# Kernel optimization log

Measured on AMD Instinct MI355X. Metric: run time of the kernel, lower is better.

## Reference

```python
import jax, jax.numpy as jnp
import numpy as np

T, H, E, I, K, G, KG = 16384, 1024, 64, 768, 8, 8, 4


def setup_inputs() -> dict:
    key = jax.random.key(0)
    ks = jax.random.split(key, 6)
    return {
        "hidden_states": jax.random.normal(ks[0], (T, H), jnp.float32),
        "gate_weight": jax.random.normal(ks[1], (E, H), jnp.float32) * 0.02,
        "correction_bias": jax.random.normal(ks[2], (E,), jnp.float32) * 0.01,
        "w_gate": jax.random.normal(ks[3], (E, I, H), jnp.float32) * 0.02,
        "w_up": jax.random.normal(ks[4], (E, I, H), jnp.float32) * 0.02,
        "w_down": jax.random.normal(ks[5], (E, H, I), jnp.float32) * 0.02,
    }


def _grouped_topk(hidden, gate_w, bias, top_k=K, n_group=G, topk_group=KG, renormalize=True):
    # gate runs in fp32 (MoEGate.dtype = float32)
    logits = hidden.astype(jnp.float32) @ gate_w.T  # [T, E]
    scores = jax.nn.sigmoid(logits)  # noaux_tc uses sigmoid scores
    s_choice = scores + bias[None, :].astype(jnp.float32)
    t, e = scores.shape
    # group score = sum of top-2 biased scores within each group
    grouped = s_choice.reshape(t, n_group, e // n_group)
    top2, _ = jax.lax.top_k(grouped, 2)
    group_scores = top2.sum(-1)  # [T, G]
    _, gidx = jax.lax.top_k(group_scores, topk_group)  # [T, KG]
    gmask = jnp.zeros((t, n_group), jnp.float32).at[jnp.arange(t)[:, None], gidx].set(1.0)
    emask = jnp.repeat(gmask, e // n_group, axis=1)  # [T, E]
    masked = jnp.where(emask > 0, s_choice, -jnp.inf)
    _, topk_idx = jax.lax.top_k(masked, top_k)  # [T, K]
    # weights use the unbiased sigmoid scores
    topk_w = jnp.take_along_axis(scores, topk_idx, axis=1)
    if renormalize:
        topk_w = topk_w / (topk_w.sum(-1, keepdims=True) + 1e-20)
    # routed_scaling_factor = 1.0
    return topk_idx, topk_w


def reference(hidden_states, gate_weight, correction_bias, w_gate, w_up, w_down):
    t = hidden_states.shape[0]
    topk_idx, topk_w = _grouped_topk(hidden_states, gate_weight, correction_bias)
    # dense combine weights [T, E]: zero except at selected experts
    combine = jnp.zeros((t, E), hidden_states.dtype).at[
        jnp.arange(t)[:, None], topk_idx
    ].add(topk_w.astype(hidden_states.dtype))

    def step(acc, xs):
        wg, wu, wd, c = xs  # wg/wu: [I,H], wd: [H,I], c: [T]
        h = jax.nn.silu(hidden_states @ wg.T) * (hidden_states @ wu.T)  # [T, I]
        return acc + c[:, None] * (h @ wd.T), None

    acc0 = jnp.zeros_like(hidden_states)
    out, _ = jax.lax.scan(step, acc0, (w_gate, w_up, w_down, combine.T))
    return out
```

## Files before the change

kernel.cpp:

```cpp
#include <hip/hip_runtime.h>
#include <hip/hip_bf16.h>
#include <math.h>

#define T_TOK 16384
#define H_DIM 1024
#define E_NUM 64
#define I_DIM 768
#define TOPK  8
#define NGRP  8
#define KGRP  4
#define S_ASN (T_TOK*TOPK)
#define BM 128
#define BK 64
#define MAXBLK (S_ASN/BM + E_NUM)

typedef __attribute__((ext_vector_type(4))) float f4v;
typedef __attribute__((ext_vector_type(8))) short s8v;
typedef __attribute__((ext_vector_type(4))) unsigned short u4sv;

#define GLDS16(g, l) __builtin_amdgcn_global_load_lds( \
    (const __attribute__((address_space(1))) void*)(g), \
    (__attribute__((address_space(3))) void*)(l), 16, 0, 0)

static __device__ __forceinline__ short f2bf(float f){
  union { float f; unsigned u; } a; a.f = f;
  unsigned u = a.u;
  unsigned r = (u + 0x7fffu + ((u >> 16) & 1u)) >> 16;
  return (short)r;
}
static __device__ __forceinline__ float bf2f(unsigned short h){
  union { unsigned u; float f; } a; a.u = ((unsigned)h) << 16; return a.f;
}
static __device__ __forceinline__ s8v cvt8(f4v a, f4v b){
  s8v r;
  r[0]=f2bf(a[0]); r[1]=f2bf(a[1]); r[2]=f2bf(a[2]); r[3]=f2bf(a[3]);
  r[4]=f2bf(b[0]); r[5]=f2bf(b[1]); r[6]=f2bf(b[2]); r[7]=f2bf(b[3]);
  return r;
}

__launch_bounds__(256)
__global__ void cast_kernel(const float* __restrict__ src,
                            short* __restrict__ dst, long n8)
{
  long i = (long)blockIdx.x*blockDim.x + threadIdx.x;
  long stride = (long)gridDim.x*blockDim.x;
  for (; i < n8; i += stride){
    f4v a = *(const f4v*)(src + i*8);
    f4v b = *(const f4v*)(src + i*8 + 4);
    *(s8v*)(dst + i*8) = cvt8(a, b);
  }
}

__launch_bounds__(256)
__global__ void gate_kernel(const float* __restrict__ hidden,
                            const float* __restrict__ gate_w,
                            double* __restrict__ logits,
                            short*  __restrict__ hb)
{
  __shared__ float sX[64][33];
  __shared__ float sW[64][33];
  const int tid  = threadIdx.x;
  const int t0   = blockIdx.x * 64;
  const int srow = tid >> 2;
  const int scol = (tid & 3) * 8;
  const int tx = tid & 15, ty = tid >> 4;
  double acc[4][4];
  #pragma unroll
  for (int i=0;i<4;i++)
    #pragma unroll
    for (int j=0;j<4;j++) acc[i][j]=0.0;

  for (int k0=0;k0<H_DIM;k0+=32){
    f4v a0 = *(const f4v*)&hidden[(size_t)(t0+srow)*H_DIM + k0 + scol];
    f4v a1 = *(const f4v*)&hidden[(size_t)(t0+srow)*H_DIM + k0 + scol + 4];
    f4v b0 = *(const f4v*)&gate_w[(size_t)srow*H_DIM + k0 + scol];
    f4v b1 = *(const f4v*)&gate_w[(size_t)srow*H_DIM + k0 + scol + 4];
    if (hb)
      *(s8v*)&hb[(size_t)(t0+srow)*H_DIM + k0 + scol] = cvt8(a0, a1);
    __syncthreads();
    #pragma unroll
    for (int j=0;j<4;j++){
      sX[srow][scol+j]   = a0[j];  sX[srow][scol+4+j] = a1[j];
      sW[srow][scol+j]   = b0[j];  sW[srow][scol+4+j] = b1[j];
    }
    __syncthreads();
    #pragma unroll
    for (int kk=0;kk<32;kk++){
      float xv[4], wv[4];
      #pragma unroll
      for (int i=0;i<4;i++){ xv[i]=sX[ty*4+i][kk]; wv[i]=sW[tx*4+i][kk]; }
      #pragma unroll
      for (int i=0;i<4;i++)
        #pragma unroll
        for (int j=0;j<4;j++)
          acc[i][j] += (double)xv[i] * (double)wv[j];
    }
  }
  #pragma unroll
  for (int i=0;i<4;i++)
    #pragma unroll
    for (int j=0;j<4;j++)
      logits[(size_t)(t0+ty*4+i)*E_NUM + tx*4+j] = acc[i][j];
}

__global__ void route_kernel(const double* __restrict__ logits,
                             const float*  __restrict__ bias,
                             int*   __restrict__ topk_idx,
                             float* __restrict__ topk_w,
                             int*   __restrict__ counts)
{
  const int t = blockIdx.x * blockDim.x + threadIdx.x;
  if (t >= T_TOK) return;
  const double* lg = logits + (size_t)t * E_NUM;
  double sc[E_NUM], sch[E_NUM];
  for (int e2=0;e2<E_NUM;e2++){
    double s = 1.0 / (1.0 + exp(-lg[e2]));
    sc[e2]  = s;
    sch[e2] = s + (double)bias[e2];
  }
  double gs[NGRP];
  for (int g=0;g<NGRP;g++){
    double m1=-1e300, m2=-1e300;
    for (int j=0;j<8;j++){
      double v = sch[g*8+j];
      if (v > m1){ m2 = m1; m1 = v; } else if (v > m2){ m2 = v; }
    }
    gs[g] = m1 + m2;
  }
  unsigned gsel = 0;
  for (int r=0;r<KGRP;r++){
    int best = 0; double bv = -1.0e308;
    for (int g=0;g<NGRP;g++)
      if (!((gsel>>g)&1u) && gs[g] > bv){ bv = gs[g]; best = g; }
    gsel |= 1u << best;
  }
  unsigned long long used = 0ULL;
  double wsum = 0.0;
  int sel[TOPK]; double w[TOPK];
  for (int r=0;r<TOPK;r++){
    int best = 0; double bv = -1.0e308;
    for (int e2=0;e2<E_NUM;e2++){
      if ((used>>e2)&1ULL) continue;
      if (!((gsel>>(e2>>3))&1u)) continue;
      if (sch[e2] > bv){ bv = sch[e2]; best = e2; }
    }
    used |= 1ULL << best;
    sel[r] = best;
    w[r]   = sc[best];
    wsum  += w[r];
  }
  double inv = 1.0 / (wsum + 1e-20);
  for (int r=0;r<TOPK;r++){
    topk_idx[(size_t)t*TOPK + r] = sel[r];
    topk_w  [(size_t)t*TOPK + r] = (float)(w[r]*inv);
    atomicAdd(&counts[sel[r]], 1);
  }
}

__global__ void scan_kernel(const int* __restrict__ counts,
                            int* __restrict__ offsets,
                            int* __restrict__ blk_start)
{
  if (threadIdx.x == 0 && blockIdx.x == 0){
    int off = 0, blk = 0;
    for (int e=0;e<E_NUM;e++){
      offsets[e] = off; blk_start[e] = blk;
      off += counts[e];
      blk += (counts[e] + BM - 1) / BM;
    }
    offsets[E_NUM] = off; blk_start[E_NUM] = blk;
  }
}

__global__ void scatter_kernel(const int* __restrict__ topk_idx,
                               const float* __restrict__ topk_w,
                               const int* __restrict__ offsets,
                               int* __restrict__ cursor,
                               int* __restrict__ token_list,
                               float* __restrict__ weight_list,
                               int* __restrict__ pos_list)
{
  const int t = blockIdx.x*blockDim.x + threadIdx.x;
  if (t >= T_TOK) return;
  for (int r=0;r<TOPK;r++){
    int   e2 = topk_idx[(size_t)t*TOPK + r];
    float wv = topk_w [(size_t)t*TOPK + r];
    int p = atomicAdd(&cursor[e2], 1);
    token_list [offsets[e2] + p] = t;
    weight_list[offsets[e2] + p] = wv;
    pos_list[(size_t)t*TOPK + r] = offsets[e2] + p;
  }
}


__launch_bounds__(512, 4)
__global__ void ffn1_fast(const short* __restrict__ hid_bf,
                          const short* __restrict__ wg_bf,
                          const short* __restrict__ wu_bf,
                          const int*   __restrict__ token_list,
                          const float* __restrict__ weight_list,
                          const int*   __restrict__ offsets,
                          const int*   __restrict__ blk_start,
                          short*       __restrict__ h_all)
{
  __shared__ short lsX[128*64];
  __shared__ short lsG[128*64];
  __shared__ short lsU[128*64];
  __shared__ float lsWt[128];

  const int bx = blockIdx.x;
  if (bx >= blk_start[E_NUM]) return;
  int e = 0;
  while (blk_start[e+1] <= bx) ++e;
  const int rb   = bx - blk_start[e];
  const int cb   = blockIdx.y;
  const int base = offsets[e];
  const int n_e  = offsets[e+1] - base;
  const int row0 = rb * BM;

  const int tid = threadIdx.x;
  const int lane = tid & 63, wid = tid >> 6;
  const int wm = wid >> 2, wn = wid & 3;
  const int l15 = lane & 15, l4 = lane >> 4;

  if (tid < BM) lsWt[tid] = ((row0+tid) < n_e) ? weight_list[base+row0+tid] : 0.f;

  const short* srcA[2];
  #pragma unroll
  for (int i=0;i<2;i++){
    int s_lin = i*512 + tid;
    int row = s_lin >> 3, sl = s_lin & 7;
    int asn = base + row0 + row; if (asn >= S_ASN) asn = S_ASN-1;
    int tok = token_list[asn];
    srcA[i] = hid_bf + (size_t)tok*H_DIM + ((sl ^ (row&7))<<3);
  }
  const short* srcG[2]; const short* srcU[2];
  #pragma unroll
  for (int i=0;i<2;i++){
    int s_lin = i*512 + tid;
    int row = s_lin >> 3, sl = s_lin & 7;
    size_t wrow = ((size_t)e*I_DIM + cb*128 + row)*H_DIM + ((sl ^ (row&7))<<3);
    srcG[i] = wg_bf + wrow;
    srcU[i] = wu_bf + wrow;
  }
  short* dstA0 = lsX + wid*512;
  short* dstG0 = lsG + wid*512;
  short* dstU0 = lsU + wid*512;

  f4v accg[4][2], accu[4][2];
  #pragma unroll
  for (int m=0;m<4;m++)
    #pragma unroll
    for (int n=0;n<2;n++){
      accg[m][n]=(f4v){0.f,0.f,0.f,0.f};
      accu[m][n]=(f4v){0.f,0.f,0.f,0.f};
    }

  for (int k0=0; k0<H_DIM; k0+=BK){
    __syncthreads();
    #pragma unroll
    for (int i=0;i<2;i++) GLDS16(srcA[i]+k0, dstA0 + i*4096);
    #pragma unroll
    for (int i=0;i<2;i++) GLDS16(srcG[i]+k0, dstG0 + i*4096);
    #pragma unroll
    for (int i=0;i<2;i++) GLDS16(srcU[i]+k0, dstU0 + i*4096);
    __syncthreads();
    #pragma unroll
    for (int kk=0;kk<2;kk++){
      s8v af[4], bg[2], bu[2];
      #pragma unroll
      for (int m=0;m<4;m++){
        int r = wm*64 + m*16 + l15;
        int s = (kk*4 + l4) ^ (r & 7);
        af[m] = *(const s8v*)&lsX[r*64 + (s<<3)];
      }
      #pragma unroll
      for (int n=0;n<2;n++){
        int r = wn*32 + n*16 + l15;
        int s = (kk*4 + l4) ^ (r & 7);
        bg[n] = *(const s8v*)&lsG[r*64 + (s<<3)];
        bu[n] = *(const s8v*)&lsU[r*64 + (s<<3)];
      }
      #pragma unroll
      for (int m=0;m<4;m++)
        #pragma unroll
        for (int n=0;n<2;n++){
          accg[m][n] = __builtin_amdgcn_mfma_f32_16x16x32_bf16(af[m], bg[n], accg[m][n], 0,0,0);
          accu[m][n] = __builtin_amdgcn_mfma_f32_16x16x32_bf16(af[m], bu[n], accu[m][n], 0,0,0);
        }
    }
  }
  #pragma unroll
  for (int m=0;m<4;m++){
    #pragma unroll
    for (int i=0;i<4;i++){
      int r = wm*64 + m*16 + l4*4 + i;
      if (row0 + r < n_e){
        float wgt = lsWt[r];
        size_t hb = (size_t)(base+row0+r)*I_DIM + (size_t)cb*128;
        #pragma unroll
        for (int n=0;n<2;n++){
          int c = wn*32 + n*16 + l15;
          float g = accg[m][n][i], u = accu[m][n][i];
          float s = g / (1.f + __expf(-g));
          h_all[hb + c] = f2bf(s * u * wgt);
        }
      }
    }
  }
}

__launch_bounds__(256, 3)
__global__ void ffn2y_fast(const short* __restrict__ h_all,
                           const short* __restrict__ wd_bf,
                           const int*   __restrict__ offsets,
                           const int*   __restrict__ blk_start,
                           short*       __restrict__ y,
                           int          cb0)
{
  __shared__ short lsA[128*64];
  __shared__ short lsB[128*64];

  const int bx = blockIdx.x;
  if (bx >= blk_start[E_NUM]) return;
  int e = 0;
  while (blk_start[e+1] <= bx) ++e;
  const int rb   = bx - blk_start[e];
  const int cby  = blockIdx.y;
  const int cbg  = cb0*4 + cby;
  const int base = offsets[e];
  const int n_e  = offsets[e+1] - base;
  const int row0 = rb * BM;

  const int tid = threadIdx.x;
  const int lane = tid & 63, wid = tid >> 6;
  const int wm = wid >> 1, wn = wid & 1;
  const int l15 = lane & 15, l4 = lane >> 4;

  const short* srcA[4]; const short* srcB[4];
  #pragma unroll
  for (int i=0;i<4;i++){
    int s_lin = i*256 + tid;
    int row = s_lin >> 3, sl = s_lin & 7;
    int arow = base + row0 + row; if (arow >= S_ASN) arow = S_ASN-1;
    srcA[i] = h_all + (size_t)arow*I_DIM + ((sl ^ (row&7))<<3);
    srcB[i] = wd_bf + ((size_t)e*H_DIM + cbg*128 + row)*I_DIM + ((sl ^ (row&7))<<3);
  }
  short* dstA0 = lsA + wid*512;
  short* dstB0 = lsB + wid*512;

  f4v acc[4][4];
  #pragma unroll
  for (int m=0;m<4;m++)
    #pragma unroll
    for (int n=0;n<4;n++) acc[m][n]=(f4v){0.f,0.f,0.f,0.f};

  for (int k0=0; k0<I_DIM; k0+=BK){
    __syncthreads();
    #pragma unroll
    for (int i=0;i<4;i++) GLDS16(srcA[i]+k0, dstA0 + i*2048);
    #pragma unroll
    for (int i=0;i<4;i++) GLDS16(srcB[i]+k0, dstB0 + i*2048);
    __syncthreads();
    #pragma unroll
    for (int kk=0;kk<2;kk++){
      s8v af[4], bf[4];
      #pragma unroll
      for (int m=0;m<4;m++){
        int r = wm*64 + m*16 + l15;
        int s = (kk*4 + l4) ^ (r & 7);
        af[m] = *(const s8v*)&lsA[r*64 + (s<<3)];
      }
      #pragma unroll
      for (int n=0;n<4;n++){
        int r = wn*64 + n*16 + l15;
        int s = (kk*4 + l4) ^ (r & 7);
        bf[n] = *(const s8v*)&lsB[r*64 + (s<<3)];
      }
      #pragma unroll
      for (int m=0;m<4;m++)
        #pragma unroll
        for (int n=0;n<4;n++)
          acc[m][n] = __builtin_amdgcn_mfma_f32_16x16x32_bf16(af[m], bf[n], acc[m][n], 0,0,0);
    }
  }
  #pragma unroll
  for (int m=0;m<4;m++){
    #pragma unroll
    for (int i=0;i<4;i++){
      int r = wm*64 + m*16 + l4*4 + i;
      if (row0 + r < n_e){
        size_t yb = (size_t)(base+row0+r)*512 + (size_t)cby*128;
        #pragma unroll
        for (int n=0;n<4;n++){
          int c = wn*64 + n*16 + l15;
          y[yb + c] = f2bf(acc[m][n][i]);
        }
      }
    }
  }
}

__launch_bounds__(256)
__global__ void combine_kernel(const short* __restrict__ y,
                               const int*   __restrict__ pos,
                               float*       __restrict__ out,
                               int cb0)
{
  const int tid = threadIdx.x;
  const int t = blockIdx.x*2 + (tid >> 7);
  const int c = (tid & 127) * 4;
  const int* pp = pos + (size_t)t*TOPK;
  float s0=0.f, s1=0.f, s2=0.f, s3=0.f;
  #pragma unroll
  for (int r=0;r<TOPK;r++){
    int row = pp[r];
    u4sv v = *(const u4sv*)&y[(size_t)row*512 + c];
    s0 += bf2f(v[0]); s1 += bf2f(v[1]); s2 += bf2f(v[2]); s3 += bf2f(v[3]);
  }
  f4v o = {s0,s1,s2,s3};
  *(f4v*)&out[(size_t)t*H_DIM + (size_t)cb0*512 + c] = o;
}

__launch_bounds__(512, 2)
__global__ void ffn1_kernel(const float* __restrict__ hidden,
                            const float* __restrict__ w_gate,
                            const float* __restrict__ w_up,
                            const int*   __restrict__ token_list,
                            const float* __restrict__ weight_list,
                            const int*   __restrict__ offsets,
                            const int*   __restrict__ blk_start,
                            short*       __restrict__ h_all)
{
  __shared__ short lsX[BM*64];
  __shared__ short lsG[BM*64];
  __shared__ short lsU[BM*64];
  __shared__ float lsWt[BM];

  const int bx = blockIdx.x;
  if (bx >= blk_start[E_NUM]) return;
  int e = 0;
  while (blk_start[e+1] <= bx) ++e;
  const int rb   = bx - blk_start[e];
  const int cb   = blockIdx.y;
  const int base = offsets[e];
  const int n_e  = offsets[e+1] - base;
  const int row0 = rb * BM;

  const int tid   = threadIdx.x;
  const int srow  = tid >> 2;
  const int scol  = (tid & 3) << 4;
  const int slot0 = (tid & 3) << 1;
  const int wsl0  = srow*64 + (((slot0  ) ^ (srow & 7)) << 3);
  const int wsl1  = srow*64 + (((slot0+1) ^ (srow & 7)) << 3);

  const bool tvalid = (row0 + srow) < n_e;
  int tok = 0;
  if (tvalid) tok = token_list[base + row0 + srow];
  const float* xsrc = hidden + (size_t)tok * H_DIM + scol;
  const size_t woff = (size_t)e * I_DIM * H_DIM + (size_t)(cb*128 + srow) * H_DIM + scol;
  const float* gsrc = w_gate + woff;
  const float* usrc = w_up   + woff;

  const int lane = tid & 63, wid = tid >> 6;
  const int wm = wid >> 2, wn = wid & 3;
  const int l15 = lane & 15, l4 = lane >> 4;

  f4v accg[4][2], accu[4][2];
  #pragma unroll
  for (int m=0;m<4;m++)
    #pragma unroll
    for (int n=0;n<2;n++){
      accg[m][n]=(f4v){0.f,0.f,0.f,0.f};
      accu[m][n]=(f4v){0.f,0.f,0.f,0.f};
    }

  for (int k0=0; k0<H_DIM; k0+=BK){
    f4v x0,x1,x2,x3;
    if (tvalid){
      x0 = *(const f4v*)(xsrc+k0);   x1 = *(const f4v*)(xsrc+k0+4);
      x2 = *(const f4v*)(xsrc+k0+8); x3 = *(const f4v*)(xsrc+k0+12);
    } else {
      x0=x1=x2=x3=(f4v){0.f,0.f,0.f,0.f};
    }
    f4v g0 = *(const f4v*)(gsrc+k0),   g1 = *(const f4v*)(gsrc+k0+4);
    f4v g2 = *(const f4v*)(gsrc+k0+8), g3 = *(const f4v*)(gsrc+k0+12);
    f4v u0 = *(const f4v*)(usrc+k0),   u1 = *(const f4v*)(usrc+k0+4);
    f4v u2 = *(const f4v*)(usrc+k0+8), u3 = *(const f4v*)(usrc+k0+12);
    __syncthreads();
    *(s8v*)&lsX[wsl0] = cvt8(x0,x1);  *(s8v*)&lsX[wsl1] = cvt8(x2,x3);
    *(s8v*)&lsG[wsl0] = cvt8(g0,g1);  *(s8v*)&lsG[wsl1] = cvt8(g2,g3);
    *(s8v*)&lsU[wsl0] = cvt8(u0,u1);  *(s8v*)&lsU[wsl1] = cvt8(u2,u3);
    __syncthreads();
    #pragma unroll
    for (int kk=0;kk<2;kk++){
      s8v af[4], bg[2], bu[2];
      #pragma unroll
      for (int m=0;m<4;m++){
        int r = wm*64 + m*16 + l15;
        int s = (kk*4 + l4) ^ (r & 7);
        af[m] = *(const s8v*)&lsX[r*64 + (s<<3)];
      }
      #pragma unroll
      for (int n=0;n<2;n++){
        int r = wn*32 + n*16 + l15;
        int s = (kk*4 + l4) ^ (r & 7);
        bg[n] = *(const s8v*)&lsG[r*64 + (s<<3)];
        bu[n] = *(const s8v*)&lsU[r*64 + (s<<3)];
      }
      #pragma unroll
      for (int m=0;m<4;m++)
        #pragma unroll
        for (int n=0;n<2;n++){
          accg[m][n] = __builtin_amdgcn_mfma_f32_16x16x32_bf16(af[m], bg[n], accg[m][n], 0,0,0);
          accu[m][n] = __builtin_amdgcn_mfma_f32_16x16x32_bf16(af[m], bu[n], accu[m][n], 0,0,0);
        }
    }
  }
  if (tid < BM) lsWt[tid] = ((row0+tid) < n_e) ? weight_list[base+row0+tid] : 0.f;
  __syncthreads();
  #pragma unroll
  for (int m=0;m<4;m++){
    #pragma unroll
    for (int i=0;i<4;i++){
      int r = wm*64 + m*16 + l4*4 + i;
      if (row0 + r < n_e){
        float wgt = lsWt[r];
        size_t hb = (size_t)(base+row0+r)*I_DIM + (size_t)cb*128;
        #pragma unroll
        for (int n=0;n<2;n++){
          int c = wn*32 + n*16 + l15;
          float g = accg[m][n][i], u = accu[m][n][i];
          float s = g / (1.f + __expf(-g));
          h_all[hb + c] = f2bf(s * u * wgt);
        }
      }
    }
  }
}

__launch_bounds__(512, 2)
__global__ void ffn2_kernel(const short* __restrict__ h_all,
                            const float* __restrict__ w_down,
                            const int*   __restrict__ token_list,
                            const int*   __restrict__ offsets,
                            const int*   __restrict__ blk_start,
                            float*       __restrict__ out)
{
  __shared__ short lsA[BM*64];
  __shared__ short lsB[BM*64];
  __shared__ int   lsT[BM];

  const int bx = blockIdx.x;
  if (bx >= blk_start[E_NUM]) return;
  int e = 0;
  while (blk_start[e+1] <= bx) ++e;
  const int rb   = bx - blk_start[e];
  const int cb   = blockIdx.y;
  const int base = offsets[e];
  const int n_e  = offsets[e+1] - base;
  const int row0 = rb * BM;

  const int tid   = threadIdx.x;
  const int srow  = tid >> 2;
  const int slot0 = (tid & 3) << 1;
  const int wsl0  = srow*64 + (((slot0  ) ^ (srow & 7)) << 3);
  const int wsl1  = srow*64 + (((slot0+1) ^ (srow & 7)) << 3);

  int arow = base + row0 + srow;
  if (arow >= S_ASN) arow = S_ASN - 1;
  const short* asrc = h_all + (size_t)arow*I_DIM + ((tid&3)<<4);
  const float* bsrc = w_down + (size_t)e*H_DIM*I_DIM
                    + (size_t)(cb*128 + srow)*I_DIM + ((tid&3)<<4);

  const int lane = tid & 63, wid = tid >> 6;
  const int wm = wid >> 2, wn = wid & 3;
  const int l15 = lane & 15, l4 = lane >> 4;

  f4v acc[4][2];
  #pragma unroll
  for (int m=0;m<4;m++)
    #pragma unroll
    for (int n=0;n<2;n++) acc[m][n]=(f4v){0.f,0.f,0.f,0.f};

  for (int k0=0; k0<I_DIM; k0+=BK){
    s8v alo = *(const s8v*)(asrc + k0);
    s8v ahi = *(const s8v*)(asrc + k0 + 8);
    f4v b0 = *(const f4v*)(bsrc+k0),   b1 = *(const f4v*)(bsrc+k0+4);
    f4v b2 = *(const f4v*)(bsrc+k0+8), b3 = *(const f4v*)(bsrc+k0+12);
    __syncthreads();
    *(s8v*)&lsA[wsl0] = alo;          *(s8v*)&lsA[wsl1] = ahi;
    *(s8v*)&lsB[wsl0] = cvt8(b0,b1);  *(s8v*)&lsB[wsl1] = cvt8(b2,b3);
    __syncthreads();
    #pragma unroll
    for (int kk=0;kk<2;kk++){
      s8v af[4], bf[2];
      #pragma unroll
      for (int m=0;m<4;m++){
        int r = wm*64 + m*16 + l15;
        int s = (kk*4 + l4) ^ (r & 7);
        af[m] = *(const s8v*)&lsA[r*64 + (s<<3)];
      }
      #pragma unroll
      for (int n=0;n<2;n++){
        int r = wn*32 + n*16 + l15;
        int s = (kk*4 + l4) ^ (r & 7);
        bf[n] = *(const s8v*)&lsB[r*64 + (s<<3)];
      }
      #pragma unroll
      for (int m=0;m<4;m++)
        #pragma unroll
        for (int n=0;n<2;n++)
          acc[m][n] = __builtin_amdgcn_mfma_f32_16x16x32_bf16(af[m], bf[n], acc[m][n], 0,0,0);
    }
  }
  if (tid < BM) lsT[tid] = ((row0+tid) < n_e) ? token_list[base+row0+tid] : -1;
  __syncthreads();
  #pragma unroll
  for (int m=0;m<4;m++){
    #pragma unroll
    for (int i=0;i<4;i++){
      int r = wm*64 + m*16 + l4*4 + i;
      int tk = lsT[r];
      if (tk >= 0){
        #pragma unroll
        for (int n=0;n<2;n++){
          int c = cb*128 + wn*32 + n*16 + l15;
          atomicAdd(&out[(size_t)tk*H_DIM + c], acc[m][n][i]);
        }
      }
    }
  }
}

extern "C" void kernel_launch(void* const* d_in, const int* in_sizes, int n_in,
                              void* d_out, int out_size, void* d_ws, size_t ws_size,
                              hipStream_t stream)
{
  const float* hidden = (const float*)d_in[0];
  const float* gate_w = (const float*)d_in[1];
  const float* bias   = (const float*)d_in[2];
  const float* w_gate = (const float*)d_in[3];
  const float* w_up   = (const float*)d_in[4];
  const float* w_down = (const float*)d_in[5];
  float* out = (float*)d_out;

  char* ws = (char*)d_ws;
  size_t off = 0;
  #define WALLOC(bytes) (ws + off); off += (((size_t)(bytes)) + 255) & ~(size_t)255
  double* logits    = (double*)WALLOC((size_t)T_TOK*E_NUM*8);
  int*    topk_idx  = (int*)   WALLOC((size_t)T_TOK*TOPK*4);
  float*  topk_w    = (float*) WALLOC((size_t)T_TOK*TOPK*4);
  int*    counts    = (int*)   WALLOC(256);
  int*    cursor    = (int*)   WALLOC(256);
  int*    offsets   = (int*)   WALLOC(512);
  int*    blk_st    = (int*)   WALLOC(512);
  int*    token_l   = (int*)   WALLOC((size_t)S_ASN*4);
  float*  weight_l  = (float*) WALLOC((size_t)S_ASN*4);
  int*    pos_l     = (int*)   WALLOC((size_t)S_ASN*4);
  short*  h_all     = (short*) WALLOC((size_t)S_ASN*I_DIM*2);
  const size_t base_need = off;
  short*  hid_bf    = (short*) WALLOC((size_t)T_TOK*H_DIM*2);
  short*  wg_bf     = (short*) WALLOC((size_t)E_NUM*I_DIM*H_DIM*2);
  short*  wu_bf     = (short*) WALLOC((size_t)E_NUM*I_DIM*H_DIM*2);
  short*  wd_bf     = (short*) WALLOC((size_t)E_NUM*H_DIM*I_DIM*2);
  const size_t fast_need = off;
  #undef WALLOC
  short* y_all = hid_bf;

  const bool fast = (ws_size >= fast_need);
  if (ws_size < base_need) return;

  hipMemsetAsync(counts, 0, 512, stream);

  gate_kernel   <<<T_TOK/64,  256, 0, stream>>>(hidden, gate_w, logits,
                                                fast ? hid_bf : (short*)0);
  route_kernel  <<<T_TOK/256, 256, 0, stream>>>(logits, bias, topk_idx, topk_w, counts);
  scan_kernel   <<<1, 64, 0, stream>>>(counts, offsets, blk_st);
  scatter_kernel<<<T_TOK/256, 256, 0, stream>>>(topk_idx, topk_w, offsets, cursor,
                                                token_l, weight_l, pos_l);
  if (fast){
    long n8w = (long)E_NUM*I_DIM*H_DIM/8;
    cast_kernel<<<3072, 256, 0, stream>>>(w_gate, wg_bf, n8w);
    cast_kernel<<<3072, 256, 0, stream>>>(w_up,   wu_bf, n8w);
    cast_kernel<<<3072, 256, 0, stream>>>(w_down, wd_bf, n8w);
    dim3 g1(MAXBLK, I_DIM/128);
    ffn1_fast<<<g1, 512, 0, stream>>>(hid_bf, wg_bf, wu_bf, token_l, weight_l,
                                      offsets, blk_st, h_all);
    dim3 g2(MAXBLK, 4);
    for (int half = 0; half < 2; ++half){
      ffn2y_fast<<<g2, 256, 0, stream>>>(h_all, wd_bf, offsets, blk_st,
                                         y_all, half);
      combine_kernel<<<T_TOK/2, 256, 0, stream>>>(y_all, pos_l, out, half);
    }
  } else {
    hipMemsetAsync(out, 0, (size_t)T_TOK*H_DIM*4, stream);
    dim3 g1(MAXBLK, I_DIM/128);
    ffn1_kernel<<<g1, 512, 0, stream>>>(hidden, w_gate, w_up, token_l, weight_l,
                                        offsets, blk_st, h_all);
    dim3 g2(MAXBLK, H_DIM/128);
    ffn2_kernel<<<g2, 512, 0, stream>>>(h_all, w_down, token_l, offsets, blk_st, out);
  }
}
```

Measured before the change: 1.703 ms.

## Schedule expert GEMM tiles by XCD with persistent loop for L2 weight reuse

The grouped FFN kernels now map work so that each XCD (blockIdx.x & 7) handles only experts congruent to it modulo 8. The scan kernel computes per-XCD block offsets for this. Tiles within an expert are ordered row-block-fastest, so blocks sharing the same weight column slice run together on one XCD's L2. The kernels become grid-stride loops over a fixed grid, which replaces the old 2D grid with its many early-exit blocks. The cost is possible load imbalance across XCDs when expert counts differ, plus a per-iteration expert lookup.

```diff
diff --git a/kernel.cpp b/kernel.cpp
--- a/kernel.cpp
+++ b/kernel.cpp
@@ -13,6 +13,10 @@
 #define BM 128
 #define BK 64
 #define MAXBLK (S_ASN/BM + E_NUM)
+#define NCB1 6
+#define NCB2 4
+#define JS1 1024
+#define JS2 768
 
 typedef __attribute__((ext_vector_type(4))) float f4v;
 typedef __attribute__((ext_vector_type(8))) short s8v;
@@ -159,16 +163,24 @@
 
 __global__ void scan_kernel(const int* __restrict__ counts,
                             int* __restrict__ offsets,
-                            int* __restrict__ blk_start)
+                            int* __restrict__ blk_start,
+                            int* __restrict__ xoff,
+                            int* __restrict__ qblk)
 {
   if (threadIdx.x == 0 && blockIdx.x == 0){
     int off = 0, blk = 0;
+    int cnt[8];
+    for (int x=0;x<8;x++) cnt[x]=0;
     for (int e=0;e<E_NUM;e++){
       offsets[e] = off; blk_start[e] = blk;
+      int nblk = (counts[e] + BM - 1) / BM;
+      xoff[e] = cnt[e & 7];
+      cnt[e & 7] += nblk;
       off += counts[e];
-      blk += (counts[e] + BM - 1) / BM;
+      blk += nblk;
     }
     offsets[E_NUM] = off; blk_start[E_NUM] = blk;
+    for (int x=0;x<8;x++) qblk[x] = cnt[x];
   }
 }
 
@@ -200,7 +212,8 @@
                           const int*   __restrict__ token_list,
                           const float* __restrict__ weight_list,
                           const int*   __restrict__ offsets,
-                          const int*   __restrict__ blk_start,
+                          const int*   __restrict__ xoff,
+                          const int*   __restrict__ qblk,
                           short*       __restrict__ h_all)
 {
   __shared__ short lsX[128*64];
@@ -208,102 +221,114 @@
   __shared__ short lsU[128*64];
   __shared__ float lsWt[128];
 
-  const int bx = blockIdx.x;
-  if (bx >= blk_start[E_NUM]) return;
-  int e = 0;
-  while (blk_start[e+1] <= bx) ++e;
-  const int rb   = bx - blk_start[e];
-  const int cb   = blockIdx.y;
-  const int base = offsets[e];
-  const int n_e  = offsets[e+1] - base;
-  const int row0 = rb * BM;
+  const int xcd = blockIdx.x & 7;
+  const int j0  = blockIdx.x >> 3;
+  const int qn  = qblk[xcd] * NCB1;
 
   const int tid = threadIdx.x;
   const int lane = tid & 63, wid = tid >> 6;
   const int wm = wid >> 2, wn = wid & 3;
   const int l15 = lane & 15, l4 = lane >> 4;
 
-  if (tid < BM) lsWt[tid] = ((row0+tid) < n_e) ? weight_list[base+row0+tid] : 0.f;
-
-  const short* srcA[2];
-  #pragma unroll
-  for (int i=0;i<2;i++){
-    int s_lin = i*512 + tid;
-    int row = s_lin >> 3, sl = s_lin & 7;
-    int asn = base + row0 + row; if (asn >= S_ASN) asn = S_ASN-1;
-    int tok = token_list[asn];
-    srcA[i] = hid_bf + (size_t)tok*H_DIM + ((sl ^ (row&7))<<3);
-  }
-  const short* srcG[2]; const short* srcU[2];
-  #pragma unroll
-  for (int i=0;i<2;i++){
-    int s_lin = i*512 + tid;
-    int row = s_lin >> 3, sl = s_lin & 7;
-    size_t wrow = ((size_t)e*I_DIM + cb*128 + row)*H_DIM + ((sl ^ (row&7))<<3);
-    srcG[i] = wg_bf + wrow;
-    srcU[i] = wu_bf + wrow;
-  }
-  short* dstA0 = lsX + wid*512;
-  short* dstG0 = lsG + wid*512;
-  short* dstU0 = lsU + wid*512;
-
-  f4v accg[4][2], accu[4][2];
-  #pragma unroll
-  for (int m=0;m<4;m++)
-    #pragma unroll
-    for (int n=0;n<2;n++){
-      accg[m][n]=(f4v){0.f,0.f,0.f,0.f};
-      accu[m][n]=(f4v){0.f,0.f,0.f,0.f};
-    }
-
-  for (int k0=0; k0<H_DIM; k0+=BK){
+  for (int j = j0; j < qn; j += JS1){
+    int e = -1, nb = 0;
+    #pragma unroll
+    for (int i=0;i<8;i++){
+      int ee  = xcd + (i<<3);
+      int nbe = (offsets[ee+1] - offsets[ee] + BM-1) >> 7;
+      int hi  = (xoff[ee] + nbe) * NCB1;
+      if (e < 0 && j < hi){ e = ee; nb = nbe; }
+    }
+    const int local = j - xoff[e]*NCB1;
+    const int cb = local / nb;
+    const int rb = local - cb*nb;
+    const int base = offsets[e];
+    const int n_e  = offsets[e+1] - base;
+    const int row0 = rb * BM;
+
     __syncthreads();
-    #pragma unroll
-    for (int i=0;i<2;i++) GLDS16(srcA[i]+k0, dstA0 + i*4096);
-    #pragma unroll
-    for (int i=0;i<2;i++) GLDS16(srcG[i]+k0, dstG0 + i*4096);
-    #pragma unroll
-    for (int i=0;i<2;i++) GLDS16(srcU[i]+k0, dstU0 + i*4096);
-    __syncthreads();
-    #pragma unroll
-    for (int kk=0;kk<2;kk++){
-      s8v af[4], bg[2], bu[2];
-      #pragma unroll
-      for (int m=0;m<4;m++){
-        int r = wm*64 + m*16 + l15;
-        int s = (kk*4 + l4) ^ (r & 7);
-        af[m] = *(const s8v*)&lsX[r*64 + (s<<3)];
-      }
+    if (tid < BM) lsWt[tid] = ((row0+tid) < n_e) ? weight_list[base+row0+tid] : 0.f;
+
+    const short* srcA[2];
+    #pragma unroll
+    for (int i=0;i<2;i++){
+      int s_lin = i*512 + tid;
+      int row = s_lin >> 3, sl = s_lin & 7;
+      int asn = base + row0 + row; if (asn >= S_ASN) asn = S_ASN-1;
+      int tok = token_list[asn];
+      srcA[i] = hid_bf + (size_t)tok*H_DIM + ((sl ^ (row&7))<<3);
+    }
+    const short* srcG[2]; const short* srcU[2];
+    #pragma unroll
+    for (int i=0;i<2;i++){
+      int s_lin = i*512 + tid;
+      int row = s_lin >> 3, sl = s_lin & 7;
+      size_t wrow = ((size_t)e*I_DIM + cb*128 + row)*H_DIM + ((sl ^ (row&7))<<3);
+      srcG[i] = wg_bf + wrow;
+      srcU[i] = wu_bf + wrow;
+    }
+    short* dstA0 = lsX + wid*512;
+    short* dstG0 = lsG + wid*512;
+    short* dstU0 = lsU + wid*512;
+
+    f4v accg[4][2], accu[4][2];
+    #pragma unroll
+    for (int m=0;m<4;m++)
       #pragma unroll
       for (int n=0;n<2;n++){
-        int r = wn*32 + n*16 + l15;
-        int s = (kk*4 + l4) ^ (r & 7);
-        bg[n] = *(const s8v*)&lsG[r*64 + (s<<3)];
-        bu[n] = *(const s8v*)&lsU[r*64 + (s<<3)];
-      }
-      #pragma unroll
-      for (int m=0;m<4;m++)
+        accg[m][n]=(f4v){0.f,0.f,0.f,0.f};
+        accu[m][n]=(f4v){0.f,0.f,0.f,0.f};
+      }
+
+    for (int k0=0; k0<H_DIM; k0+=BK){
+      __syncthreads();
+      #pragma unroll
+      for (int i=0;i<2;i++) GLDS16(srcA[i]+k0, dstA0 + i*4096);
+      #pragma unroll
+      for (int i=0;i<2;i++) GLDS16(srcG[i]+k0, dstG0 + i*4096);
+      #pragma unroll
+      for (int i=0;i<2;i++) GLDS16(srcU[i]+k0, dstU0 + i*4096);
+      __syncthreads();
+      #pragma unroll
+      for (int kk=0;kk<2;kk++){
+        s8v af[4], bg[2], bu[2];
+        #pragma unroll
+        for (int m=0;m<4;m++){
+          int r = wm*64 + m*16 + l15;
+          int s = (kk*4 + l4) ^ (r & 7);
+          af[m] = *(const s8v*)&lsX[r*64 + (s<<3)];
+        }
         #pragma unroll
         for (int n=0;n<2;n++){
-          accg[m][n] = __builtin_amdgcn_mfma_f32_16x16x32_bf16(af[m], bg[n], accg[m][n], 0,0,0);
-          accu[m][n] = __builtin_amdgcn_mfma_f32_16x16x32_bf16(af[m], bu[n], accu[m][n], 0,0,0);
-        }
-    }
-  }
-  #pragma unroll
-  for (int m=0;m<4;m++){
-    #pragma unroll
-    for (int i=0;i<4;i++){
-      int r = wm*64 + m*16 + l4*4 + i;
-      if (row0 + r < n_e){
-        float wgt = lsWt[r];
-        size_t hb = (size_t)(base+row0+r)*I_DIM + (size_t)cb*128;
-        #pragma unroll
-        for (int n=0;n<2;n++){
-          int c = wn*32 + n*16 + l15;
-          float g = accg[m][n][i], u = accu[m][n][i];
-          float s = g / (1.f + __expf(-g));
-          h_all[hb + c] = f2bf(s * u * wgt);
+          int r = wn*32 + n*16 + l15;
+          int s = (kk*4 + l4) ^ (r & 7);
+          bg[n] = *(const s8v*)&lsG[r*64 + (s<<3)];
+          bu[n] = *(const s8v*)&lsU[r*64 + (s<<3)];
+        }
+        #pragma unroll
+        for (int m=0;m<4;m++)
+          #pragma unroll
+          for (int n=0;n<2;n++){
+            accg[m][n] = __builtin_amdgcn_mfma_f32_16x16x32_bf16(af[m], bg[n], accg[m][n], 0,0,0);
+            accu[m][n] = __builtin_amdgcn_mfma_f32_16x16x32_bf16(af[m], bu[n], accu[m][n], 0,0,0);
+          }
+      }
+    }
+    #pragma unroll
+    for (int m=0;m<4;m++){
+      #pragma unroll
+      for (int i=0;i<4;i++){
+        int r = wm*64 + m*16 + l4*4 + i;
+        if (row0 + r < n_e){
+          float wgt = lsWt[r];
+          size_t hb = (size_t)(base+row0+r)*I_DIM + (size_t)cb*128;
+          #pragma unroll
+          for (int n=0;n<2;n++){
+            int c = wn*32 + n*16 + l15;
+            float g = accg[m][n][i], u = accu[m][n][i];
+            float s = g / (1.f + __expf(-g));
+            h_all[hb + c] = f2bf(s * u * wgt);
+          }
         }
       }
     }
@@ -314,87 +339,101 @@
 __global__ void ffn2y_fast(const short* __restrict__ h_all,
                            const short* __restrict__ wd_bf,
                            const int*   __restrict__ offsets,
-                           const int*   __restrict__ blk_start,
+                           const int*   __restrict__ xoff,
+                           const int*   __restrict__ qblk,
                            short*       __restrict__ y,
                            int          cb0)
 {
   __shared__ short lsA[128*64];
   __shared__ short lsB[128*64];
 
-  const int bx = blockIdx.x;
-  if (bx >= blk_start[E_NUM]) return;
-  int e = 0;
-  while (blk_start[e+1] <= bx) ++e;
-  const int rb   = bx - blk_start[e];
-  const int cby  = blockIdx.y;
-  const int cbg  = cb0*4 + cby;
-  const int base = offsets[e];
-  const int n_e  = offsets[e+1] - base;
-  const int row0 = rb * BM;
+  const int xcd = blockIdx.x & 7;
+  const int j0  = blockIdx.x >> 3;
+  const int qn  = qblk[xcd] * NCB2;
 
   const int tid = threadIdx.x;
   const int lane = tid & 63, wid = tid >> 6;
   const int wm = wid >> 1, wn = wid & 1;
   const int l15 = lane & 15, l4 = lane >> 4;
 
-  const short* srcA[4]; const short* srcB[4];
-  #pragma unroll
-  for (int i=0;i<4;i++){
-    int s_lin = i*256 + tid;
-    int row = s_lin >> 3, sl = s_lin & 7;
-    int arow = base + row0 + row; if (arow >= S_ASN) arow = S_ASN-1;
-    srcA[i] = h_all + (size_t)arow*I_DIM + ((sl ^ (row&7))<<3);
-    srcB[i] = wd_bf + ((size_t)e*H_DIM + cbg*128 + row)*I_DIM + ((sl ^ (row&7))<<3);
-  }
-  short* dstA0 = lsA + wid*512;
-  short* dstB0 = lsB + wid*512;
-
-  f4v acc[4][4];
-  #pragma unroll
-  for (int m=0;m<4;m++)
-    #pragma unroll
-    for (int n=0;n<4;n++) acc[m][n]=(f4v){0.f,0.f,0.f,0.f};
-
-  for (int k0=0; k0<I_DIM; k0+=BK){
+  for (int j = j0; j < qn; j += JS2){
+    int e = -1, nb = 0;
+    #pragma unroll
+    for (int i=0;i<8;i++){
+      int ee  = xcd + (i<<3);
+      int nbe = (offsets[ee+1] - offsets[ee] + BM-1) >> 7;
+      int hi  = (xoff[ee] + nbe) * NCB2;
+      if (e < 0 && j < hi){ e = ee; nb = nbe; }
+    }
+    const int local = j - xoff[e]*NCB2;
+    const int cby = local / nb;
+    const int rb  = local - cby*nb;
+    const int cbg = cb0*4 + cby;
+    const int base = offsets[e];
+    const int n_e  = offsets[e+1] - base;
+    const int row0 = rb * BM;
+
     __syncthreads();
-    #pragma unroll
-    for (int i=0;i<4;i++) GLDS16(srcA[i]+k0, dstA0 + i*2048);
-    #pragma unroll
-    for (int i=0;i<4;i++) GLDS16(srcB[i]+k0, dstB0 + i*2048);
-    __syncthreads();
-    #pragma unroll
-    for (int kk=0;kk<2;kk++){
-      s8v af[4], bf[4];
-      #pragma unroll
-      for (int m=0;m<4;m++){
-        int r = wm*64 + m*16 + l15;
-        int s = (kk*4 + l4) ^ (r & 7);
-        af[m] = *(const s8v*)&lsA[r*64 + (s<<3)];
-      }
-      #pragma unroll
-      for (int n=0;n<4;n++){
-        int r = wn*64 + n*16 + l15;
-        int s = (kk*4 + l4) ^ (r & 7);
-        bf[n] = *(const s8v*)&lsB[r*64 + (s<<3)];
-      }
-      #pragma unroll
-      for (int m=0;m<4;m++)
-        #pragma unroll
-        for (int n=0;n<4;n++)
-          acc[m][n] = __builtin_amdgcn_mfma_f32_16x16x32_bf16(af[m], bf[n], acc[m][n], 0,0,0);
-    }
-  }
-  #pragma unroll
-  for (int m=0;m<4;m++){
+
+    const short* srcA[4]; const short* srcB[4];
     #pragma unroll
     for (int i=0;i<4;i++){
-      int r = wm*64 + m*16 + l4*4 + i;
-      if (row0 + r < n_e){
-        size_t yb = (size_t)(base+row0+r)*512 + (size_t)cby*128;
+      int s_lin = i*256 + tid;
+      int row = s_lin >> 3, sl = s_lin & 7;
+      int arow = base + row0 + row; if (arow >= S_ASN) arow = S_ASN-1;
+      srcA[i] = h_all + (size_t)arow*I_DIM + ((sl ^ (row&7))<<3);
+      srcB[i] = wd_bf + ((size_t)e*H_DIM + cbg*128 + row)*I_DIM + ((sl ^ (row&7))<<3);
+    }
+    short* dstA0 = lsA + wid*512;
+    short* dstB0 = lsB + wid*512;
+
+    f4v acc[4][4];
+    #pragma unroll
+    for (int m=0;m<4;m++)
+      #pragma unroll
+      for (int n=0;n<4;n++) acc[m][n]=(f4v){0.f,0.f,0.f,0.f};
+
+    for (int k0=0; k0<I_DIM; k0+=BK){
+      __syncthreads();
+      #pragma unroll
+      for (int i=0;i<4;i++) GLDS16(srcA[i]+k0, dstA0 + i*2048);
+      #pragma unroll
+      for (int i=0;i<4;i++) GLDS16(srcB[i]+k0, dstB0 + i*2048);
+      __syncthreads();
+      #pragma unroll
+      for (int kk=0;kk<2;kk++){
+        s8v af[4], bf[4];
+        #pragma unroll
+        for (int m=0;m<4;m++){
+          int r = wm*64 + m*16 + l15;
+          int s = (kk*4 + l4) ^ (r & 7);
+          af[m] = *(const s8v*)&lsA[r*64 + (s<<3)];
+        }
         #pragma unroll
         for (int n=0;n<4;n++){
-          int c = wn*64 + n*16 + l15;
-          y[yb + c] = f2bf(acc[m][n][i]);
+          int r = wn*64 + n*16 + l15;
+          int s = (kk*4 + l4) ^ (r & 7);
+          bf[n] = *(const s8v*)&lsB[r*64 + (s<<3)];
+        }
+        #pragma unroll
+        for (int m=0;m<4;m++)
+          #pragma unroll
+          for (int n=0;n<4;n++)
+            acc[m][n] = __builtin_amdgcn_mfma_f32_16x16x32_bf16(af[m], bf[n], acc[m][n], 0,0,0);
+      }
+    }
+    #pragma unroll
+    for (int m=0;m<4;m++){
+      #pragma unroll
+      for (int i=0;i<4;i++){
+        int r = wm*64 + m*16 + l4*4 + i;
+        if (row0 + r < n_e){
+          size_t yb = (size_t)(base+row0+r)*512 + (size_t)cby*128;
+          #pragma unroll
+          for (int n=0;n<4;n++){
+            int c = wn*64 + n*16 + l15;
+            y[yb + c] = f2bf(acc[m][n][i]);
+          }
         }
       }
     }
@@ -655,6 +694,8 @@
   int*    cursor    = (int*)   WALLOC(256);
   int*    offsets   = (int*)   WALLOC(512);
   int*    blk_st    = (int*)   WALLOC(512);
+  int*    xoff      = (int*)   WALLOC(256);
+  int*    qblk      = (int*)   WALLOC(256);
   int*    token_l   = (int*)   WALLOC((size_t)S_ASN*4);
   float*  weight_l  = (float*) WALLOC((size_t)S_ASN*4);
   int*    pos_l     = (int*)   WALLOC((size_t)S_ASN*4);
@@ -676,7 +717,7 @@
   gate_kernel   <<<T_TOK/64,  256, 0, stream>>>(hidden, gate_w, logits,
                                                 fast ? hid_bf : (short*)0);
   route_kernel  <<<T_TOK/256, 256, 0, stream>>>(logits, bias, topk_idx, topk_w, counts);
-  scan_kernel   <<<1, 64, 0, stream>>>(counts, offsets, blk_st);
+  scan_kernel   <<<1, 64, 0, stream>>>(counts, offsets, blk_st, xoff, qblk);
   scatter_kernel<<<T_TOK/256, 256, 0, stream>>>(topk_idx, topk_w, offsets, cursor,
                                                 token_l, weight_l, pos_l);
   if (fast){
@@ -684,13 +725,11 @@
     cast_kernel<<<3072, 256, 0, stream>>>(w_gate, wg_bf, n8w);
     cast_kernel<<<3072, 256, 0, stream>>>(w_up,   wu_bf, n8w);
     cast_kernel<<<3072, 256, 0, stream>>>(w_down, wd_bf, n8w);
-    dim3 g1(MAXBLK, I_DIM/128);
-    ffn1_fast<<<g1, 512, 0, stream>>>(hid_bf, wg_bf, wu_bf, token_l, weight_l,
-                                      offsets, blk_st, h_all);
-    dim3 g2(MAXBLK, 4);
+    ffn1_fast<<<8*JS1, 512, 0, stream>>>(hid_bf, wg_bf, wu_bf, token_l, weight_l,
+                                         offsets, xoff, qblk, h_all);
     for (int half = 0; half < 2; ++half){
-      ffn2y_fast<<<g2, 256, 0, stream>>>(h_all, wd_bf, offsets, blk_st,
-                                         y_all, half);
+      ffn2y_fast<<<8*JS2, 256, 0, stream>>>(h_all, wd_bf, offsets, xoff, qblk,
+                                            y_all, half);
       combine_kernel<<<T_TOK/2, 256, 0, stream>>>(y_all, pos_l, out, half);
     }
   } else {
```

After: 2.054 ms. 1.21x slower.
